# Kernel tuning notes

Measured on AMD Instinct MI355X. Metric: run time of the kernel, lower is better.

## Reference

```python
import jax, jax.numpy as jnp
import numpy as np

B, CH, H, W, D = 2, 32, 256, 512, 192


def setup_inputs() -> dict:
    key = jax.random.key(0)
    ks = jax.random.split(key, 10)
    def w(k, shape, fan_in):
        return jax.random.normal(k, shape, jnp.float32) * (1.0 / np.sqrt(fan_in))
    return {
        "x": jax.random.normal(ks[0], (B, CH, H, W), jnp.float32),
        "y": jax.random.normal(ks[1], (B, CH, H, W), jnp.float32),
        # encoder: 1x1 convs ch->64->32->1 (shared for x and y)
        "w1": w(ks[2], (64, CH), CH), "b1": w(ks[3], (64,), CH),
        "w2": w(ks[4], (32, 64), 64), "b2": w(ks[5], (32,), 64),
        "w3": w(ks[6], (1, 32), 32), "b3": w(ks[7], (1,), 32),
        # decoderl: 1x1 conv maxdisp->maxdisp (original code applies decoderl to BOTH volumes)
        "wd": w(ks[8], (D, D), D), "bd": w(ks[9], (D,), D),
    }


def _conv1x1(w, b, h):  # [O,C] x [B,C,H,W] -> [B,O,H,W]
    return jnp.einsum("oc,bchw->bohw", w, h) + b[None, :, None, None]


def _encoder(x, w1, b1, w2, b2, w3, b3):
    h = jax.nn.relu(x)
    h = jax.nn.relu(_conv1x1(w1, b1, h))
    h = jax.nn.relu(_conv1x1(w2, b2, h))
    h = jax.nn.relu(_conv1x1(w3, b3, h))
    return h[:, 0]  # squeeze channel -> [B,H,W]


def _cost_volumes(xf, yf):
    # costx[b,d,h,w] = xf[b,h,w+d] * yf[b,h,w]   (0 where w+d >= W)
    # costy[b,d,h,w] = xf[b,h,w]   * yf[b,h,w-d] (0 where w-d < 0)
    dgrid = jnp.arange(D)
    wgrid = jnp.arange(W)
    x_pad = jnp.pad(xf, ((0, 0), (0, 0), (0, D)))          # zero pad right
    xg = x_pad[:, :, wgrid[None, :] + dgrid[:, None]]       # [B,H,D,W]
    costx = (xg * yf[:, :, None, :]).transpose(0, 2, 1, 3)  # [B,D,H,W]
    y_pad = jnp.pad(yf, ((0, 0), (0, 0), (D, 0)))           # zero pad left
    yg = y_pad[:, :, wgrid[None, :] - dgrid[:, None] + D]   # [B,H,D,W]
    costy = (xf[:, :, None, :] * yg).transpose(0, 2, 1, 3)  # [B,D,H,W]
    return costx, costy


def reference(x, y, w1, b1, w2, b2, w3, b3, wd, bd):
    xf = _encoder(x, w1, b1, w2, b2, w3, b3)
    yf = _encoder(y, w1, b1, w2, b2, w3, b3)
    costx, costy = _cost_volumes(xf, yf)
    probx = jax.nn.softmax(_conv1x1(wd, bd, costx), axis=1)
    proby = jax.nn.softmax(_conv1x1(wd, bd, costy), axis=1)  # decoderl used for both, as in source
    disp_vals = jnp.arange(D, dtype=probx.dtype)
    dispx = jnp.einsum("bdhw,d->bhw", probx, disp_vals)
    dispy = jnp.einsum("bdhw,d->bhw", proby, disp_vals)
    return dispx, dispy
```

## Files before the change

### kernel.cpp

```cpp
#include <hip/hip_runtime.h>


typedef __attribute__((ext_vector_type(8))) __bf16 bf16x8;
typedef __attribute__((ext_vector_type(4))) float  f32x4;

#define MFMA16x16x32(a,b,c) __builtin_amdgcn_mfma_f32_16x16x32_bf16((a),(b),(c),0,0,0)

constexpr int CH = 32, HH = 256, WW = 512, DD = 192;
constexpr int HW  = HH * WW;
constexpr int CHW = CH * HW;
constexpr int OUTPLANE = 2 * HH * WW;

constexpr int WD_OFF  = 0;
constexpr int WD_SZ   = 192 * 384;
constexpr int CPS     = 1424;
constexpr int XC_OFF  = WD_OFF + WD_SZ;
constexpr int YC_OFF  = XC_OFF + 8 * CPS;
constexpr int SCY_OFF = YC_OFF + 8 * CPS;
constexpr int SCX_OFF = SCY_OFF + 2048;
constexpr int BD_OFF  = SCX_OFF + 2048;
constexpr int LDS_BYTES = BD_OFF + 768;

__global__ __launch_bounds__(512)
__attribute__((amdgpu_waves_per_eu(2, 2)))
void panet_fused(const float* __restrict__ gx,  const float* __restrict__ gy,
                 const float* __restrict__ gw1, const float* __restrict__ gb1,
                 const float* __restrict__ gw2, const float* __restrict__ gb2,
                 const float* __restrict__ gw3, const float* __restrict__ gb3,
                 const float* __restrict__ gwd, const float* __restrict__ gbd,
                 float* __restrict__ gout)
{
  extern __shared__ __align__(16) char lds[];
  const int tid  = threadIdx.x;
  const int bh   = blockIdx.x;
  const int b    = bh >> 8;
  const int h    = bh & 255;
  const int lane = tid & 63;
  const int m    = lane & 15;
  const int g    = lane >> 4;
  const int wid  = tid >> 6;

  {
    int* zp = (int*)(lds + XC_OFF);
    #pragma unroll 4
    for (int i = tid; i < (16 * CPS) / 4; i += 512) zp[i] = 0;

    unsigned short* wds = (unsigned short*)(lds + WD_OFF);
    for (int i = tid; i < 192 * 192; i += 512) {
      const int o = i / 192;
      const int k = i - o * 192;
      const __bf16 v = (__bf16)gwd[i];
      const int byt = o * 384 + ((2 * k) ^ ((o & 7) << 4));
      wds[byt >> 1] = __builtin_bit_cast(unsigned short, v);
    }
    float* bds = (float*)(lds + BD_OFF);
    if (tid < 192) bds[tid] = gbd[tid];
  }
  __syncthreads();

  {
    bf16x8 A1[4], A2[2][2];
    f32x4  bias1[4], bias2[2], w3v[2];
    #pragma unroll
    for (int Mt = 0; Mt < 4; ++Mt) {
      const float* p = gw1 + (16 * Mt + m) * 32 + 4 * g;
      const f32x4 u0 = *(const f32x4*)p;
      const f32x4 u1 = *(const f32x4*)(p + 16);
      #pragma unroll
      for (int j = 0; j < 4; ++j) { A1[Mt][j] = (__bf16)u0[j]; A1[Mt][j + 4] = (__bf16)u1[j]; }
      bias1[Mt] = *(const f32x4*)(gb1 + 16 * Mt + 4 * g);
    }
    #pragma unroll
    for (int Mt = 0; Mt < 2; ++Mt) {
      #pragma unroll
      for (int s = 0; s < 2; ++s) {
        const float* p = gw2 + (16 * Mt + m) * 64 + 32 * s + 4 * g;
        const f32x4 u0 = *(const f32x4*)p;
        const f32x4 u1 = *(const f32x4*)(p + 16);
        #pragma unroll
        for (int j = 0; j < 4; ++j) { A2[Mt][s][j] = (__bf16)u0[j]; A2[Mt][s][j + 4] = (__bf16)u1[j]; }
      }
      bias2[Mt] = *(const f32x4*)(gb2 + 16 * Mt + 4 * g);
      w3v[Mt]   = *(const f32x4*)(gw3 + 16 * Mt + 4 * g);
    }
    const float b3s = gb3[0];
    const f32x4 zf4 = {0.f, 0.f, 0.f, 0.f};

    for (int u = wid; u < 64; u += 8) {
      const int t  = u >> 5;
      const int w0 = (u & 31) << 4;
      const float* src = (t ? gy : gx) + b * CHW + h * WW + w0 + m;

      bf16x8 B1;
      #pragma unroll
      for (int j = 0; j < 8; ++j) {
        const int c = 16 * (j >> 2) + 4 * g + (j & 3);
        B1[j] = (__bf16)fmaxf(src[c * HW], 0.f);
      }
      f32x4 acc1[4];
      #pragma unroll
      for (int Mt = 0; Mt < 4; ++Mt) acc1[Mt] = MFMA16x16x32(A1[Mt], B1, zf4);

      bf16x8 B2[2];
      #pragma unroll
      for (int s = 0; s < 2; ++s) {
        #pragma unroll
        for (int j = 0; j < 4; ++j) {
          B2[s][j]     = (__bf16)fmaxf(acc1[2 * s][j]     + bias1[2 * s][j],     0.f);
          B2[s][j + 4] = (__bf16)fmaxf(acc1[2 * s + 1][j] + bias1[2 * s + 1][j], 0.f);
        }
      }
      f32x4 acc2[2];
      #pragma unroll
      for (int Mt = 0; Mt < 2; ++Mt)
        acc2[Mt] = MFMA16x16x32(A2[Mt][1], B2[1], MFMA16x16x32(A2[Mt][0], B2[0], zf4));

      float s3 = 0.f;
      #pragma unroll
      for (int Mt = 0; Mt < 2; ++Mt)
        #pragma unroll
        for (int r = 0; r < 4; ++r)
          s3 += w3v[Mt][r] * fmaxf(acc2[Mt][r] + bias2[Mt][r], 0.f);
      s3 += __shfl_xor(s3, 16);
      s3 += __shfl_xor(s3, 32);
      const float val = fmaxf(s3 + b3s, 0.f);

      if (lane < 16) {
        const int px = w0 + m;
        const unsigned short bits = __builtin_bit_cast(unsigned short, (__bf16)val);
        if (t == 0) {
          ((float*)(lds + SCX_OFF))[px] = val;
          #pragma unroll
          for (int c = 0; c < 8; ++c) {
            const int e = px - c;
            if (e >= 0) ((unsigned short*)(lds + XC_OFF + c * CPS))[e] = bits;
          }
        } else {
          ((float*)(lds + SCY_OFF))[px] = val;
          #pragma unroll
          for (int c = 0; c < 8; ++c) {
            const int e = 511 - px - c;
            if (e >= 0) ((unsigned short*)(lds + YC_OFF + c * CPS))[e] = bits;
          }
        }
      }
    }
  }
  __syncthreads();

  {
    const int dir      = wid >> 2;
    const int colbase  = (wid & 3) << 7;
    const char* Bb     = lds + (dir ? YC_OFF : XC_OFF);
    const float* scrow = (const float*)(lds + (dir ? SCX_OFF : SCY_OFF));
    float* outp = gout + dir * OUTPLANE + (((b << 8) + h) << 9);
    const int Xm   = (m & 7) << 4;
    const int arow = m * 384;
    const float g4 = 4.0f * (float)g;

    for (int chunk = 0; chunk < 4; ++chunk) {
      const int n0 = colbase + (chunk << 5);
      int   laneB[2];
      float sc[2];
      #pragma unroll
      for (int nt = 0; nt < 2; ++nt) {
        const int wc = n0 + 16 * nt + m;
        const int I0 = dir ? (511 - wc) : wc;
        const int c  = I0 & 7;
        laneB[nt] = c * CPS + 2 * (I0 - c) + 16 * g;
        sc[nt] = scrow[wc];
      }
      bf16x8 bfr[6][2];
      #pragma unroll
      for (int ks = 0; ks < 6; ++ks) {
        bfr[ks][0] = *(const bf16x8*)(Bb + laneB[0] + (ks << 6));
        bfr[ks][1] = *(const bf16x8*)(Bb + laneB[1] + (ks << 6));
      }

      float mx0 = -3.4e38f, mx1 = -3.4e38f;
      float s0 = 0.f, s1 = 0.f, ws0 = 0.f, ws1 = 0.f;

      #pragma unroll 2
      for (int mp = 0; mp < 6; ++mp) {
        f32x4 a00 = {0,0,0,0}, a01 = {0,0,0,0}, a10 = {0,0,0,0}, a11 = {0,0,0,0};
        #pragma unroll
        for (int ks = 0; ks < 6; ++ks) {
          const int inner = ((ks << 6) + (g << 4)) ^ Xm;
          const char* ap = lds + WD_OFF + (mp * 2) * 6144 + arow + inner;
          const bf16x8 af0 = *(const bf16x8*)(ap);
          const bf16x8 af1 = *(const bf16x8*)(ap + 6144);
          a00 = MFMA16x16x32(af0, bfr[ks][0], a00);
          a01 = MFMA16x16x32(af0, bfr[ks][1], a01);
          a10 = MFMA16x16x32(af1, bfr[ks][0], a10);
          a11 = MFMA16x16x32(af1, bfr[ks][1], a11);
        }
        const f32x4 bd0 = *(const f32x4*)(lds + BD_OFF + (mp * 2) * 64 + 16 * g);
        const f32x4 bd1 = *(const f32x4*)(lds + BD_OFF + (mp * 2 + 1) * 64 + 16 * g);
        const float ob = (float)(32 * mp);

        {
          f32x4 L0, L1;
          #pragma unroll
          for (int r = 0; r < 4; ++r) {
            L0[r] = fmaf(sc[0], a00[r], bd0[r]);
            L1[r] = fmaf(sc[0], a10[r], bd1[r]);
          }
          const float pm = fmaxf(fmaxf(fmaxf(L0[0], L0[1]), fmaxf(L0[2], L0[3])),
                                 fmaxf(fmaxf(L1[0], L1[1]), fmaxf(L1[2], L1[3])));
          const float nm = fmaxf(mx0, pm);
          const float f  = __expf(mx0 - nm);
          float ls = 0.f, lw = 0.f;
          #pragma unroll
          for (int r = 0; r < 4; ++r) {
            const float p0 = __expf(L0[r] - nm);
            const float p1 = __expf(L1[r] - nm);
            ls += p0 + p1;
            lw += (ob + (float)r) * p0 + (ob + 16.f + (float)r) * p1;
          }
          s0  = fmaf(s0,  f, ls);
          ws0 = fmaf(ws0, f, lw);
          mx0 = nm;
        }
        {
          f32x4 L0, L1;
          #pragma unroll
          for (int r = 0; r < 4; ++r) {
            L0[r] = fmaf(sc[1], a01[r], bd0[r]);
            L1[r] = fmaf(sc[1], a11[r], bd1[r]);
          }
          const float pm = fmaxf(fmaxf(fmaxf(L0[0], L0[1]), fmaxf(L0[2], L0[3])),
                                 fmaxf(fmaxf(L1[0], L1[1]), fmaxf(L1[2], L1[3])));
          const float nm = fmaxf(mx1, pm);
          const float f  = __expf(mx1 - nm);
          float ls = 0.f, lw = 0.f;
          #pragma unroll
          for (int r = 0; r < 4; ++r) {
            const float p0 = __expf(L0[r] - nm);
            const float p1 = __expf(L1[r] - nm);
            ls += p0 + p1;
            lw += (ob + (float)r) * p0 + (ob + 16.f + (float)r) * p1;
          }
          s1  = fmaf(s1,  f, ls);
          ws1 = fmaf(ws1, f, lw);
          mx1 = nm;
        }
      }

      #pragma unroll
      for (int nt = 0; nt < 2; ++nt) {
        const float mx = nt ? mx1 : mx0;
        const float s  = nt ? s1  : s0;
        const float ws = nt ? ws1 : ws0;
        float M = fmaxf(mx, __shfl_xor(mx, 16));
        M = fmaxf(M, __shfl_xor(M, 32));
        const float f = __expf(mx - M);
        float sr = s * f;
        float wr = (ws + g4 * s) * f;
        sr += __shfl_xor(sr, 16); sr += __shfl_xor(sr, 32);
        wr += __shfl_xor(wr, 16); wr += __shfl_xor(wr, 32);
        if (lane < 16) outp[n0 + 16 * nt + m] = wr / sr;
      }
    }
  }
}

extern "C" void kernel_launch(void* const* d_in, const int* in_sizes, int n_in,
                              void* d_out, int out_size, void* d_ws, size_t ws_size,
                              hipStream_t stream) {
  const float* x  = (const float*)d_in[0];
  const float* y  = (const float*)d_in[1];
  const float* w1 = (const float*)d_in[2];
  const float* b1 = (const float*)d_in[3];
  const float* w2 = (const float*)d_in[4];
  const float* b2 = (const float*)d_in[5];
  const float* w3 = (const float*)d_in[6];
  const float* b3 = (const float*)d_in[7];
  const float* wd = (const float*)d_in[8];
  const float* bd = (const float*)d_in[9];

  (void)hipFuncSetAttribute((const void*)panet_fused,
                            hipFuncAttributeMaxDynamicSharedMemorySize, LDS_BYTES);
  panet_fused<<<512, 512, LDS_BYTES, stream>>>(x, y, w1, b1, w2, b2, w3, b3, wd, bd,
                                               (float*)d_out);
}
```

Before: 91.03 us.

## Shrink shifted feature copies to two parity planes and use exp2 softmax

Replaces the eight byte-offset-shifted bf16 copies of each feature row with two parity-shifted copies. The B fragments are loaded with 4-byte-aligned dword loads instead of 16-byte vector loads, which shrinks the initial zero-fill and the LDS stores in the encoder stage. The separate fp32 scale rows are dropped and the scale is read from the bf16 copies instead, which lowers the precision of the scale factor. Bias and scale are pre-multiplied by log2(e) so the softmax can use exp2 directly, at the cost of more LDS load instructions per fragment.

```diff
diff --git a/kernel.cpp b/kernel.cpp
--- a/kernel.cpp
+++ b/kernel.cpp
@@ -3,22 +3,22 @@
 
 typedef __attribute__((ext_vector_type(8))) __bf16 bf16x8;
 typedef __attribute__((ext_vector_type(4))) float  f32x4;
+typedef __attribute__((ext_vector_type(4))) int    i32x4;
 
 #define MFMA16x16x32(a,b,c) __builtin_amdgcn_mfma_f32_16x16x32_bf16((a),(b),(c),0,0,0)
 
-constexpr int CH = 32, HH = 256, WW = 512, DD = 192;
-constexpr int HW  = HH * WW;
-constexpr int CHW = CH * HW;
-constexpr int OUTPLANE = 2 * HH * WW;
+constexpr int WW  = 512;
+constexpr int HW  = 256 * 512;
+constexpr int CHW = 32 * HW;
+constexpr int OUTPLANE = 2 * 256 * 512;
+constexpr float LOG2E = 1.4426950408889634f;
 
 constexpr int WD_OFF  = 0;
 constexpr int WD_SZ   = 192 * 384;
 constexpr int CPS     = 1424;
 constexpr int XC_OFF  = WD_OFF + WD_SZ;
-constexpr int YC_OFF  = XC_OFF + 8 * CPS;
-constexpr int SCY_OFF = YC_OFF + 8 * CPS;
-constexpr int SCX_OFF = SCY_OFF + 2048;
-constexpr int BD_OFF  = SCX_OFF + 2048;
+constexpr int YC_OFF  = XC_OFF + 2 * CPS;
+constexpr int BD_OFF  = YC_OFF + 2 * CPS;
 constexpr int LDS_BYTES = BD_OFF + 768;
 
 __global__ __launch_bounds__(512)
@@ -42,8 +42,7 @@
 
   {
     int* zp = (int*)(lds + XC_OFF);
-    #pragma unroll 4
-    for (int i = tid; i < (16 * CPS) / 4; i += 512) zp[i] = 0;
+    for (int i = tid; i < (4 * CPS) / 4; i += 512) zp[i] = 0;
 
     unsigned short* wds = (unsigned short*)(lds + WD_OFF);
     for (int i = tid; i < 192 * 192; i += 512) {
@@ -54,7 +53,7 @@
       wds[byt >> 1] = __builtin_bit_cast(unsigned short, v);
     }
     float* bds = (float*)(lds + BD_OFF);
-    if (tid < 192) bds[tid] = gbd[tid];
+    if (tid < 192) bds[tid] = gbd[tid] * LOG2E;
   }
   __syncthreads();
 
@@ -129,16 +128,14 @@
         const int px = w0 + m;
         const unsigned short bits = __builtin_bit_cast(unsigned short, (__bf16)val);
         if (t == 0) {
-          ((float*)(lds + SCX_OFF))[px] = val;
-          #pragma unroll
-          for (int c = 0; c < 8; ++c) {
+          #pragma unroll
+          for (int c = 0; c < 2; ++c) {
             const int e = px - c;
             if (e >= 0) ((unsigned short*)(lds + XC_OFF + c * CPS))[e] = bits;
           }
         } else {
-          ((float*)(lds + SCY_OFF))[px] = val;
-          #pragma unroll
-          for (int c = 0; c < 8; ++c) {
+          #pragma unroll
+          for (int c = 0; c < 2; ++c) {
             const int e = 511 - px - c;
             if (e >= 0) ((unsigned short*)(lds + YC_OFF + c * CPS))[e] = bits;
           }
@@ -152,7 +149,7 @@
     const int dir      = wid >> 2;
     const int colbase  = (wid & 3) << 7;
     const char* Bb     = lds + (dir ? YC_OFF : XC_OFF);
-    const float* scrow = (const float*)(lds + (dir ? SCX_OFF : SCY_OFF));
+    const char* scB    = lds + (dir ? XC_OFF : YC_OFF);
     float* outp = gout + dir * OUTPLANE + (((b << 8) + h) << 9);
     const int Xm   = (m & 7) << 4;
     const int arow = m * 384;
@@ -166,15 +163,20 @@
       for (int nt = 0; nt < 2; ++nt) {
         const int wc = n0 + 16 * nt + m;
         const int I0 = dir ? (511 - wc) : wc;
-        const int c  = I0 & 7;
+        const int c  = I0 & 1;
         laneB[nt] = c * CPS + 2 * (I0 - c) + 16 * g;
-        sc[nt] = scrow[wc];
+        const int sidx = dir ? wc : (511 - wc);
+        sc[nt] = LOG2E * (float)(((const __bf16*)scB)[sidx]);
       }
       bf16x8 bfr[6][2];
       #pragma unroll
       for (int ks = 0; ks < 6; ++ks) {
-        bfr[ks][0] = *(const bf16x8*)(Bb + laneB[0] + (ks << 6));
-        bfr[ks][1] = *(const bf16x8*)(Bb + laneB[1] + (ks << 6));
+        #pragma unroll
+        for (int nt = 0; nt < 2; ++nt) {
+          const int* bp = (const int*)(Bb + laneB[nt] + (ks << 6));
+          i32x4 q = { bp[0], bp[1], bp[2], bp[3] };
+          bfr[ks][nt] = __builtin_bit_cast(bf16x8, q);
+        }
       }
 
       float mx0 = -3.4e38f, mx1 = -3.4e38f;
@@ -208,12 +210,12 @@
           const float pm = fmaxf(fmaxf(fmaxf(L0[0], L0[1]), fmaxf(L0[2], L0[3])),
                                  fmaxf(fmaxf(L1[0], L1[1]), fmaxf(L1[2], L1[3])));
           const float nm = fmaxf(mx0, pm);
-          const float f  = __expf(mx0 - nm);
+          const float f  = exp2f(mx0 - nm);
           float ls = 0.f, lw = 0.f;
           #pragma unroll
           for (int r = 0; r < 4; ++r) {
-            const float p0 = __expf(L0[r] - nm);
-            const float p1 = __expf(L1[r] - nm);
+            const float p0 = exp2f(L0[r] - nm);
+            const float p1 = exp2f(L1[r] - nm);
             ls += p0 + p1;
             lw += (ob + (float)r) * p0 + (ob + 16.f + (float)r) * p1;
           }
@@ -231,12 +233,12 @@
           const float pm = fmaxf(fmaxf(fmaxf(L0[0], L0[1]), fmaxf(L0[2], L0[3])),
                                  fmaxf(fmaxf(L1[0], L1[1]), fmaxf(L1[2], L1[3])));
           const float nm = fmaxf(mx1, pm);
-          const float f  = __expf(mx1 - nm);
+          const float f  = exp2f(mx1 - nm);
           float ls = 0.f, lw = 0.f;
           #pragma unroll
           for (int r = 0; r < 4; ++r) {
-            const float p0 = __expf(L0[r] - nm);
-            const float p1 = __expf(L1[r] - nm);
+            const float p0 = exp2f(L0[r] - nm);
+            const float p1 = exp2f(L1[r] - nm);
             ls += p0 + p1;
             lw += (ob + (float)r) * p0 + (ob + 16.f + (float)r) * p1;
           }
@@ -253,7 +255,7 @@
         const float ws = nt ? ws1 : ws0;
         float M = fmaxf(mx, __shfl_xor(mx, 16));
         M = fmaxf(M, __shfl_xor(M, 32));
-        const float f = __expf(mx - M);
+        const float f = exp2f(mx - M);
         float sr = s * f;
         float wr = (ws + g4 * s) * f;
         sr += __shfl_xor(sr, 16); sr += __shfl_xor(sr, 32);
```

After: 100.2 us. 10.1% more time.
